# Kernel optimization log

Hardware: AMD Instinct MI355X
Metric: run time of the kernel (lower is better)

Reference implementation:

```python
import jax, jax.numpy as jnp
import numpy as np

LN_EPS = 1e-12  # BertLayerNorm default


def _digcn_forward(hidden_state, adjacency_matrix, Wl, bl, Ws, bs, Wr, br, ln_w, ln_b):
    B, S, D = hidden_state.shape
    temper = jnp.asarray(D, jnp.float32) ** 0.5
    i = jnp.arange(S)
    upper = (i[None, :] > i[:, None]).astype(hidden_state.dtype)  # strict upper: j > i
    lower = (i[None, :] < i[:, None]).astype(hidden_state.dtype)  # strict lower: j < i

    def layer(h, params):
        wl, b_l, ws, b_s, wr, b_r, g, beta = params
        # directed graph attention: softmax over full scores, then mask by adjacency and renormalize
        u = jnp.einsum('bid,bjd->bij', h, h) / temper            # [B,S,S]
        a = jax.nn.softmax(u, axis=-1)
        delta = a * adjacency_matrix
        attn = delta / (jnp.sum(delta, axis=-1, keepdims=True) + 1e-10)
        # three projections (torch Linear: x @ W.T + b)
        hl = h @ wl.T + b_l
        hs = h @ ws.T + b_s
        hr = h @ wr.T + b_r
        # split attention into strictly-upper (left), diagonal (self), strictly-lower (right)
        diag_a = jnp.diagonal(attn, axis1=1, axis2=2)            # [B,S]
        ctx = (jnp.einsum('bij,bjd->bid', attn * upper, hl)
               + diag_a[..., None] * hs
               + jnp.einsum('bij,bjd->bid', attn * lower, hr))
        # BertLayerNorm
        mean = ctx.mean(-1, keepdims=True)
        var = ctx.var(-1, keepdims=True)
        o = (ctx - mean) / jnp.sqrt(var + LN_EPS) * g + beta
        return jax.nn.relu(o), None

    out, _ = jax.lax.scan(layer, hidden_state, (Wl, bl, Ws, bs, Wr, br, ln_w, ln_b))
    return out


def setup_inputs() -> dict:
    key = jax.random.key(0)
    ks = jax.random.split(key, 6)
    B, S, D, L = 8, 1024, 768, 2
    scale = (1.0 / D) ** 0.5  # ~xavier scale for [D,D] linears
    hidden_state = jax.random.normal(ks[0], (B, S, D), jnp.float32)
    adjacency_matrix = (jax.random.uniform(ks[1], (B, S, S)) < 0.05).astype(jnp.float32)
    Wl = jax.random.normal(ks[2], (L, D, D), jnp.float32) * scale
    Ws = jax.random.normal(ks[3], (L, D, D), jnp.float32) * scale
    Wr = jax.random.normal(ks[4], (L, D, D), jnp.float32) * scale
    bl = jnp.zeros((L, D), jnp.float32)
    bs = jnp.zeros((L, D), jnp.float32)
    br = jnp.zeros((L, D), jnp.float32)
    ln_w = jnp.ones((L, D), jnp.float32)
    ln_b = jnp.zeros((L, D), jnp.float32)
    return dict(hidden_state=hidden_state, adjacency_matrix=adjacency_matrix,
                Wl=Wl, bl=bl, Ws=Ws, bs=bs, Wr=Wr, br=br, ln_w=ln_w, ln_b=ln_b)


def reference(hidden_state, adjacency_matrix, Wl, bl, Ws, bs, Wr, br, ln_w, ln_b):
    return _digcn_forward(hidden_state, adjacency_matrix, Wl, bl, Ws, bs, Wr, br, ln_w, ln_b)
```

## Files before the change

kernel.cpp:

```cpp
#include <hip/hip_runtime.h>
#include <hip/hip_bf16.h>


using bf16 = __hip_bfloat16;
typedef __attribute__((ext_vector_type(8))) short short8;
typedef __attribute__((ext_vector_type(4))) float f32x4;

#define B_ 8
#define S_ 1024
#define D_ 768
#define BS_ 8192
#define SS_ 1048576L
#define SD_ 786432L
#define DD_ 589824L

__device__ __forceinline__ void gload16(const void* g, void* l) {
  __builtin_amdgcn_global_load_lds((const __attribute__((address_space(1))) void*)g,
                                   (__attribute__((address_space(3))) void*)l, 16, 0, 0);
}

__device__ __forceinline__ f32x4 mfma16(short8 a, short8 b, f32x4 c) {
  return __builtin_amdgcn_mfma_f32_16x16x32_bf16(a, b, c, 0, 0, 0);
}

__device__ __forceinline__ float wave_sum(float v) {
  #pragma unroll
  for (int o = 32; o; o >>= 1) v += __shfl_xor(v, o);
  return v;
}

__device__ __forceinline__ void stage_tile(const bf16* g, long ld, int kt, short* s,
                                           int w, int lane) {
  #pragma unroll
  for (int i = 0; i < 4; ++i) {
    int rt = w * 32 + i * 8 + (lane >> 3);
    int ch = lane & 7;
    const bf16* src = g + (long)rt * ld + (long)kt * 64 + ((ch ^ (rt & 7)) << 3);
    gload16((const void*)src, (void*)(s + (w * 32 + i * 8) * 64));
  }
}

__device__ __forceinline__ short8 read_frag(const short* s, int r0, int kk, int lane) {
  int r = r0 + (lane & 15);
  int c = (kk << 2) + (lane >> 4);
  return *(const short8*)((const char*)s + r * 128 + ((c ^ (r & 7)) << 4));
}

__device__ __forceinline__ void compute_tile(const short* As, const short* Bs,
                                             f32x4 acc[4][4], int lane, int wm, int wn) {
  #pragma unroll
  for (int kk = 0; kk < 2; ++kk) {
    short8 af[4], bfr[4];
    #pragma unroll
    for (int m = 0; m < 4; ++m) af[m] = read_frag(As, wm * 64 + m * 16, kk, lane);
    #pragma unroll
    for (int n = 0; n < 4; ++n) bfr[n] = read_frag(Bs, wn * 64 + n * 16, kk, lane);
    #pragma unroll
    for (int m = 0; m < 4; ++m)
      #pragma unroll
      for (int n = 0; n < 4; ++n)
        acc[m][n] = mfma16(af[m], bfr[n], acc[m][n]);
  }
}

__device__ __forceinline__ void gemm_db(const bf16* A, long lda, const bf16* Bm, long ldb,
                                        int kt0, int kt1, short (*L)[8192],
                                        f32x4 acc[4][4], int w, int lane, int wm, int wn) {
  stage_tile(A, lda, kt0, L[0], w, lane);
  stage_tile(Bm, ldb, kt0, L[1], w, lane);
  asm volatile("s_waitcnt vmcnt(0)");
  __syncthreads();
  int cur = 0;
  for (int kt = kt0; kt < kt1; ++kt) {
    if (kt + 1 < kt1) {
      stage_tile(A, lda, kt + 1, L[2 * (cur ^ 1)], w, lane);
      stage_tile(Bm, ldb, kt + 1, L[2 * (cur ^ 1) + 1], w, lane);
    }
    compute_tile(L[2 * cur], L[2 * cur + 1], acc, lane, wm, wn);
    asm volatile("s_waitcnt vmcnt(0)");
    __syncthreads();
    cur ^= 1;
  }
}

__global__ __launch_bounds__(256) void k_scores(const bf16* __restrict__ hb,
                                                const float* __restrict__ adj,
                                                bf16* __restrict__ paU,
                                                bf16* __restrict__ paL,
                                                float* __restrict__ diagpa,
                                                float* __restrict__ Sm,
                                                float* __restrict__ Zs,
                                                float scale) {
  __shared__ short L[4][8192];
  int b = blockIdx.z;
  int tid = threadIdx.x, w = tid >> 6, lane = tid & 63, wm = w >> 1, wn = w & 1;
  const bf16* A = hb + (long)b * SD_ + (long)blockIdx.x * 128 * D_;
  const bf16* Bp = hb + (long)b * SD_ + (long)blockIdx.y * 128 * D_;
  f32x4 acc[4][4] = {};
  gemm_db(A, D_, Bp, D_, 0, 12, L, acc, w, lane, wm, wn);
  int row0 = blockIdx.x * 128 + wm * 64, col0 = blockIdx.y * 128 + wn * 64;
  #pragma unroll
  for (int m = 0; m < 4; ++m) {
    int rbase = row0 + m * 16 + ((lane >> 4) << 2);
    #pragma unroll
    for (int j = 0; j < 4; ++j) {
      int rs = rbase + j;
      long rowg = (long)b * S_ + rs;
      float psum = 0.f, pasum = 0.f;
      #pragma unroll
      for (int n = 0; n < 4; ++n) {
        int cs = col0 + n * 16 + (lane & 15);
        float p = __expf(acc[m][n][j] * scale);
        float a = adj[rowg * S_ + cs];
        bf16 pb = __float2bfloat16(p * a);
        float pa = __bfloat162float(pb);
        psum += p; pasum += pa;
        paU[rowg * S_ + cs] = (cs > rs) ? pb : __float2bfloat16(0.f);
        paL[rowg * S_ + cs] = (cs < rs) ? pb : __float2bfloat16(0.f);
        if (cs == rs) diagpa[rowg] = pa;
      }
      #pragma unroll
      for (int o = 1; o < 16; o <<= 1) {
        psum += __shfl_xor(psum, o);
        pasum += __shfl_xor(pasum, o);
      }
      if ((lane & 15) == 0) {
        atomicAdd(&Sm[rowg], pasum);
        atomicAdd(&Zs[rowg], psum);
      }
    }
  }
}

__global__ __launch_bounds__(256) void k_proj(const bf16* __restrict__ hb,
                                              const bf16* __restrict__ Wb,
                                              const float* __restrict__ bl,
                                              const float* __restrict__ bs,
                                              const float* __restrict__ br,
                                              bf16* __restrict__ hlT,
                                              bf16* __restrict__ hsb,
                                              bf16* __restrict__ hrT) {
  __shared__ short L[4][8192];
  int z = blockIdx.z;
  int tid = threadIdx.x, w = tid >> 6, lane = tid & 63, wm = w >> 1, wn = w & 1;
  const bf16* A = hb + (long)blockIdx.x * 128 * D_;
  const bf16* Bp = Wb + (long)z * 2 * DD_ + (long)blockIdx.y * 128 * D_;
  f32x4 acc[4][4] = {};
  gemm_db(A, D_, Bp, D_, 0, 12, L, acc, w, lane, wm, wn);
  const float* bias = (z == 0) ? bl : (z == 1) ? bs : br;
  int row0 = blockIdx.x * 128 + wm * 64, col0 = blockIdx.y * 128 + wn * 64;
  if (z == 1) {
    #pragma unroll
    for (int m = 0; m < 4; ++m) {
      int r = row0 + m * 16 + ((lane >> 4) << 2);
      #pragma unroll
      for (int n = 0; n < 4; ++n) {
        int c = col0 + n * 16 + (lane & 15);
        float bv = bias[c];
        #pragma unroll
        for (int j = 0; j < 4; ++j)
          hsb[(long)(r + j) * D_ + c] = __float2bfloat16(acc[m][n][j] + bv);
      }
    }
  } else {
    bf16* outT = (z == 0) ? hlT : hrT;
    #pragma unroll
    for (int m = 0; m < 4; ++m) {
      int r = row0 + m * 16 + ((lane >> 4) << 2);
      #pragma unroll
      for (int n = 0; n < 4; ++n) {
        int c = col0 + n * 16 + (lane & 15);
        float bv = bias[c];
        #pragma unroll
        for (int j = 0; j < 4; ++j)
          outT[(long)c * BS_ + r + j] = __float2bfloat16(acc[m][n][j] + bv);
      }
    }
  }
}

__global__ __launch_bounds__(256) void k_ctx(const bf16* __restrict__ paU,
                                             const bf16* __restrict__ paL,
                                             const bf16* __restrict__ hlT,
                                             const bf16* __restrict__ hrT,
                                             const bf16* __restrict__ hsb,
                                             const float* __restrict__ diagpa,
                                             const float* __restrict__ Sm,
                                             const float* __restrict__ Zs,
                                             float* __restrict__ ctx) {
  __shared__ short L[4][8192];
  int b = blockIdx.z;
  int tid = threadIdx.x, w = tid >> 6, lane = tid & 63, wm = w >> 1, wn = w & 1;
  int rm = blockIdx.x * 128;
  int t = rm >> 6;
  const bf16* A1 = paU + (long)b * SS_ + (long)rm * S_;
  const bf16* B1 = hlT + (long)blockIdx.y * 128 * BS_ + (long)b * S_;
  const bf16* A2 = paL + (long)b * SS_ + (long)rm * S_;
  const bf16* B2 = hrT + (long)blockIdx.y * 128 * BS_ + (long)b * S_;
  int ntU = 16 - t;
  int nt = ntU + t + 2;
  f32x4 acc[4][4] = {};

  const bf16 *Ap, *Bp; int kt;
  {
    Ap = A1; Bp = B1; kt = t;
    stage_tile(Ap, S_, kt, L[0], w, lane);
    stage_tile(Bp, BS_, kt, L[1], w, lane);
  }
  asm volatile("s_waitcnt vmcnt(0)");
  __syncthreads();
  int cur = 0;
  for (int q = 0; q < nt; ++q) {
    if (q + 1 < nt) {
      int qn = q + 1;
      if (qn < ntU) { Ap = A1; Bp = B1; kt = t + qn; }
      else          { Ap = A2; Bp = B2; kt = qn - ntU; }
      stage_tile(Ap, S_, kt, L[2 * (cur ^ 1)], w, lane);
      stage_tile(Bp, BS_, kt, L[2 * (cur ^ 1) + 1], w, lane);
    }
    compute_tile(L[2 * cur], L[2 * cur + 1], acc, lane, wm, wn);
    asm volatile("s_waitcnt vmcnt(0)");
    __syncthreads();
    cur ^= 1;
  }

  int row0 = rm + wm * 64, col0 = blockIdx.y * 128 + wn * 64;
  #pragma unroll
  for (int m = 0; m < 4; ++m) {
    int r = row0 + m * 16 + ((lane >> 4) << 2);
    float dg[4], inv[4];
    #pragma unroll
    for (int j = 0; j < 4; ++j) {
      long gr = (long)b * S_ + r + j;
      dg[j] = diagpa[gr];
      inv[j] = 1.0f / (Sm[gr] + 1e-10f * Zs[gr]);
    }
    #pragma unroll
    for (int n = 0; n < 4; ++n) {
      int c = col0 + n * 16 + (lane & 15);
      #pragma unroll
      for (int j = 0; j < 4; ++j) {
        long gr = (long)b * S_ + r + j;
        float hv = __bfloat162float(hsb[gr * D_ + c]);
        ctx[gr * D_ + c] = (acc[m][n][j] + dg[j] * hv) * inv[j];
      }
    }
  }
}

__global__ __launch_bounds__(256) void k_ln(const float* __restrict__ ctx,
                                            const float* __restrict__ g,
                                            const float* __restrict__ beta,
                                            float* __restrict__ outF,
                                            bf16* __restrict__ outB) {
  int wv = threadIdx.x >> 6, lane = threadIdx.x & 63;
  long row = (long)blockIdx.x * 4 + wv;
  const float* x = ctx + row * D_;
  float v[12]; float s = 0.f;
  #pragma unroll
  for (int k = 0; k < 12; ++k) { v[k] = x[k * 64 + lane]; s += v[k]; }
  s = wave_sum(s);
  float mean = s * (1.0f / 768.0f);
  float q = 0.f;
  #pragma unroll
  for (int k = 0; k < 12; ++k) { float d = v[k] - mean; q += d * d; }
  q = wave_sum(q);
  float inv = rsqrtf(fmaxf(q * (1.0f / 768.0f), 0.f) + 1e-12f);
  #pragma unroll
  for (int k = 0; k < 12; ++k) {
    int c = k * 64 + lane;
    float o = fmaxf((v[k] - mean) * inv * g[c] + beta[c], 0.f);
    if (outF) outF[row * D_ + c] = o;
    if (outB) outB[row * D_ + c] = __float2bfloat16(o);
  }
}

__global__ __launch_bounds__(256) void k_castf(const float* __restrict__ in,
                                               bf16* __restrict__ out) {
  long idx = ((long)blockIdx.x * 256 + threadIdx.x) * 4;
  float4 f = *(const float4*)(in + idx);
  out[idx] = __float2bfloat16(f.x);
  out[idx + 1] = __float2bfloat16(f.y);
  out[idx + 2] = __float2bfloat16(f.z);
  out[idx + 3] = __float2bfloat16(f.w);
}

__global__ __launch_bounds__(256) void k_castw(const float* __restrict__ wl,
                                               const float* __restrict__ ws_,
                                               const float* __restrict__ wr,
                                               bf16* __restrict__ out) {
  const float* src = (blockIdx.y == 0) ? wl : (blockIdx.y == 1) ? ws_ : wr;
  bf16* o = out + (long)blockIdx.y * 2 * DD_;
  long idx = ((long)blockIdx.x * 256 + threadIdx.x) * 4;
  float4 f = *(const float4*)(src + idx);
  o[idx] = __float2bfloat16(f.x);
  o[idx + 1] = __float2bfloat16(f.y);
  o[idx + 2] = __float2bfloat16(f.z);
  o[idx + 3] = __float2bfloat16(f.w);
}

extern "C" void kernel_launch(void* const* d_in, const int* in_sizes, int n_in,
                              void* d_out, int out_size, void* d_ws, size_t ws_size,
                              hipStream_t stream) {
  const float* hidden = (const float*)d_in[0];
  const float* adj    = (const float*)d_in[1];
  const float* Wl     = (const float*)d_in[2];
  const float* bl     = (const float*)d_in[3];
  const float* Ws     = (const float*)d_in[4];
  const float* bs     = (const float*)d_in[5];
  const float* Wr     = (const float*)d_in[6];
  const float* br     = (const float*)d_in[7];
  const float* lnw    = (const float*)d_in[8];
  const float* lnb    = (const float*)d_in[9];
  float* out = (float*)d_out;

  char* ws = (char*)d_ws;
  bf16*  hb     = (bf16*)(ws);
  bf16*  hlT    = (bf16*)(ws + 12582912);
  bf16*  hrT    = (bf16*)(ws + 25165824);
  bf16*  hsb    = (bf16*)(ws + 37748736);
  bf16*  Wb     = (bf16*)(ws + 50331648);
  float* diagpa = (float*)(ws + 57409536);
  float* SmZ    = (float*)(ws + 57442304);
  bf16*  paU    = (bf16*)(ws + 57507840);
  bf16*  paL    = (bf16*)(ws + 74285056);
  float* ctx    = (float*)(ws + 91062272);

  float* Sm = SmZ;
  float* Zs = SmZ + BS_;
  const float scale = 0.03608439182435161f;

  k_castf<<<6144, 256, 0, stream>>>(hidden, hb);
  k_castw<<<dim3(1152, 3), 256, 0, stream>>>(Wl, Ws, Wr, Wb);
  for (int l = 0; l < 2; ++l) {
    hipMemsetAsync(SmZ, 0, 2 * BS_ * sizeof(float), stream);
    k_scores<<<dim3(8, 8, B_), 256, 0, stream>>>(hb, adj, paU, paL, diagpa, Sm, Zs, scale);
    k_proj<<<dim3(64, 6, 3), 256, 0, stream>>>(hb, Wb + (long)l * DD_, bl + l * D_,
                                               bs + l * D_, br + l * D_, hlT, hsb, hrT);
    k_ctx<<<dim3(8, 6, B_), 256, 0, stream>>>(paU, paL, hlT, hrT, hsb, diagpa, Sm, Zs, ctx);
    k_ln<<<2048, 256, 0, stream>>>(ctx, lnw + l * D_, lnb + l * D_,
                                   (l == 1) ? out : nullptr,
                                   (l == 1) ? (bf16*)nullptr : hb);
  }
}
```

Before: 351.5 us.

## Bit-pack adjacency, merge masked attention buffers, drop row normalization, stage stores through LDS

A new kernel packs the float adjacency matrix into a bitmask once per call, and both layers reuse it. This replaces the float adjacency reads in the scores kernel. The scores kernel now writes one shared attention matrix, and only the diagonal 128x128 blocks get separate upper and lower copies. This replaces two full-size masked matrices. The per-row renormalization sums, their atomics and the memset are removed, because LayerNorm is invariant to a positive per-row scale; this leaves only a tiny epsilon difference. Output tiles in the scores and projection kernels are staged through shared memory so global stores, including the transposed ones, are coalesced 16-byte writes.

After: 353.9 us. Within noise of the previous version (+0.7%).

```diff
diff --git a/kernel.cpp b/kernel.cpp
--- a/kernel.cpp
+++ b/kernel.cpp
@@ -27,6 +27,11 @@
   #pragma unroll
   for (int o = 32; o; o >>= 1) v += __shfl_xor(v, o);
   return v;
+}
+
+__device__ __forceinline__ short bfbits(float x) {
+  bf16 h = __float2bfloat16(x);
+  return *reinterpret_cast<short*>(&h);
 }
 
 __device__ __forceinline__ void stage_tile(const bf16* g, long ld, int kt, short* s,
@@ -83,52 +88,79 @@
   }
 }
 
+__device__ __forceinline__ void copy_out(const short* T, short* dst, long ldg, int tid) {
+  #pragma unroll
+  for (int q = 0; q < 8; ++q) {
+    int id = q * 256 + tid;
+    int r = id >> 4, chk = id & 15;
+    short8 v = *(const short8*)(T + r * 136 + chk * 8);
+    *(short8*)(dst + (long)r * ldg + chk * 8) = v;
+  }
+}
+
+__global__ __launch_bounds__(256) void k_packadj(const float* __restrict__ adj,
+                                                 unsigned long long* __restrict__ am) {
+  int gw = (blockIdx.x * 256 + threadIdx.x) >> 6;
+  int lane = threadIdx.x & 63;
+  for (int it = 0; it < 64; ++it) {
+    long base = ((long)(it * 2048 + gw)) * 64;
+    float v = adj[base + lane];
+    unsigned long long b = __ballot(v != 0.0f);
+    if (lane == 0) am[base >> 6] = b;
+  }
+}
+
 __global__ __launch_bounds__(256) void k_scores(const bf16* __restrict__ hb,
-                                                const float* __restrict__ adj,
-                                                bf16* __restrict__ paU,
-                                                bf16* __restrict__ paL,
+                                                const unsigned* __restrict__ am,
+                                                bf16* __restrict__ pa,
+                                                bf16* __restrict__ paUb,
+                                                bf16* __restrict__ paLb,
                                                 float* __restrict__ diagpa,
-                                                float* __restrict__ Sm,
-                                                float* __restrict__ Zs,
                                                 float scale) {
   __shared__ short L[4][8192];
-  int b = blockIdx.z;
+  int b = blockIdx.z, bx = blockIdx.x, by = blockIdx.y;
   int tid = threadIdx.x, w = tid >> 6, lane = tid & 63, wm = w >> 1, wn = w & 1;
-  const bf16* A = hb + (long)b * SD_ + (long)blockIdx.x * 128 * D_;
-  const bf16* Bp = hb + (long)b * SD_ + (long)blockIdx.y * 128 * D_;
+  const bf16* A = hb + (long)b * SD_ + (long)bx * 128 * D_;
+  const bf16* Bp = hb + (long)b * SD_ + (long)by * 128 * D_;
   f32x4 acc[4][4] = {};
   gemm_db(A, D_, Bp, D_, 0, 12, L, acc, w, lane, wm, wn);
-  int row0 = blockIdx.x * 128 + wm * 64, col0 = blockIdx.y * 128 + wn * 64;
-  #pragma unroll
-  for (int m = 0; m < 4; ++m) {
-    int rbase = row0 + m * 16 + ((lane >> 4) << 2);
-    #pragma unroll
-    for (int j = 0; j < 4; ++j) {
-      int rs = rbase + j;
-      long rowg = (long)b * S_ + rs;
-      float psum = 0.f, pasum = 0.f;
+  bool dgb = (bx == by);
+  short* T = (short*)L;
+  int row0 = wm * 64, col0 = wn * 64;
+  int rs_off = bx * 128, cs_off = by * 128;
+  int npass = dgb ? 2 : 1;
+  for (int pass = 0; pass < npass; ++pass) {
+    if (pass) __syncthreads();
+    #pragma unroll
+    for (int m = 0; m < 4; ++m) {
+      int rl0 = row0 + m * 16 + ((lane >> 4) << 2);
       #pragma unroll
-      for (int n = 0; n < 4; ++n) {
-        int cs = col0 + n * 16 + (lane & 15);
-        float p = __expf(acc[m][n][j] * scale);
-        float a = adj[rowg * S_ + cs];
-        bf16 pb = __float2bfloat16(p * a);
-        float pa = __bfloat162float(pb);
-        psum += p; pasum += pa;
-        paU[rowg * S_ + cs] = (cs > rs) ? pb : __float2bfloat16(0.f);
-        paL[rowg * S_ + cs] = (cs < rs) ? pb : __float2bfloat16(0.f);
-        if (cs == rs) diagpa[rowg] = pa;
+      for (int j = 0; j < 4; ++j) {
+        int rl = rl0 + j;
+        int rglob = rs_off + rl;
+        long rowg = (long)b * S_ + rglob;
+        const unsigned* mrow = am + rowg * 32 + (cs_off >> 5) + (wn << 1);
+        unsigned w0 = mrow[0], w1 = mrow[1];
+        #pragma unroll
+        for (int n = 0; n < 4; ++n) {
+          int cl = col0 + n * 16 + (lane & 15);
+          int cglob = cs_off + cl;
+          unsigned wv = (n & 2) ? w1 : w0;
+          int bit = (wv >> (((n & 1) << 4) + (lane & 15))) & 1;
+          float p = __expf(acc[m][n][j] * scale);
+          float pav = bit ? p : 0.f;
+          if (dgb && pass == 0 && cglob == rglob) diagpa[rowg] = pav;
+          bool keep = !dgb || (pass == 0 ? (cglob > rglob) : (cglob < rglob));
+          T[rl * 136 + cl] = bfbits(keep ? pav : 0.f);
+        }
       }
-      #pragma unroll
-      for (int o = 1; o < 16; o <<= 1) {
-        psum += __shfl_xor(psum, o);
-        pasum += __shfl_xor(pasum, o);
-      }
-      if ((lane & 15) == 0) {
-        atomicAdd(&Sm[rowg], pasum);
-        atomicAdd(&Zs[rowg], psum);
-      }
-    }
+    }
+    __syncthreads();
+    short* dst; long ldg;
+    if (!dgb)           { dst = (short*)pa   + (long)b * SS_ + (long)rs_off * S_ + cs_off; ldg = S_; }
+    else if (pass == 0) { dst = (short*)paUb + (long)b * (S_ * 128L) + (long)rs_off * 128; ldg = 128; }
+    else                { dst = (short*)paLb + (long)b * (S_ * 128L) + (long)rs_off * 128; ldg = 128; }
+    copy_out(T, dst, ldg, tid);
   }
 }
 
@@ -148,75 +180,77 @@
   f32x4 acc[4][4] = {};
   gemm_db(A, D_, Bp, D_, 0, 12, L, acc, w, lane, wm, wn);
   const float* bias = (z == 0) ? bl : (z == 1) ? bs : br;
-  int row0 = blockIdx.x * 128 + wm * 64, col0 = blockIdx.y * 128 + wn * 64;
+  int rowg0 = blockIdx.x * 128, colg0 = blockIdx.y * 128;
+  short* T = (short*)L;
+  #pragma unroll
+  for (int m = 0; m < 4; ++m) {
+    int rl0 = wm * 64 + m * 16 + ((lane >> 4) << 2);
+    #pragma unroll
+    for (int n = 0; n < 4; ++n) {
+      int cl = wn * 64 + n * 16 + (lane & 15);
+      float bv = bias[colg0 + cl];
+      #pragma unroll
+      for (int j = 0; j < 4; ++j) {
+        short v = bfbits(acc[m][n][j] + bv);
+        if (z == 1) T[(rl0 + j) * 136 + cl] = v;
+        else        T[cl * 136 + rl0 + j] = v;
+      }
+    }
+  }
+  __syncthreads();
   if (z == 1) {
-    #pragma unroll
-    for (int m = 0; m < 4; ++m) {
-      int r = row0 + m * 16 + ((lane >> 4) << 2);
-      #pragma unroll
-      for (int n = 0; n < 4; ++n) {
-        int c = col0 + n * 16 + (lane & 15);
-        float bv = bias[c];
-        #pragma unroll
-        for (int j = 0; j < 4; ++j)
-          hsb[(long)(r + j) * D_ + c] = __float2bfloat16(acc[m][n][j] + bv);
-      }
-    }
+    copy_out(T, (short*)hsb + (long)rowg0 * D_ + colg0, D_, tid);
   } else {
-    bf16* outT = (z == 0) ? hlT : hrT;
-    #pragma unroll
-    for (int m = 0; m < 4; ++m) {
-      int r = row0 + m * 16 + ((lane >> 4) << 2);
-      #pragma unroll
-      for (int n = 0; n < 4; ++n) {
-        int c = col0 + n * 16 + (lane & 15);
-        float bv = bias[c];
-        #pragma unroll
-        for (int j = 0; j < 4; ++j)
-          outT[(long)c * BS_ + r + j] = __float2bfloat16(acc[m][n][j] + bv);
-      }
-    }
-  }
-}
-
-__global__ __launch_bounds__(256) void k_ctx(const bf16* __restrict__ paU,
-                                             const bf16* __restrict__ paL,
+    short* outT = (short*)((z == 0) ? hlT : hrT);
+    copy_out(T, outT + (long)colg0 * BS_ + rowg0, BS_, tid);
+  }
+}
+
+__global__ __launch_bounds__(256) void k_ctx(const bf16* __restrict__ pa,
+                                             const bf16* __restrict__ paUb,
+                                             const bf16* __restrict__ paLb,
                                              const bf16* __restrict__ hlT,
                                              const bf16* __restrict__ hrT,
                                              const bf16* __restrict__ hsb,
                                              const float* __restrict__ diagpa,
-                                             const float* __restrict__ Sm,
-                                             const float* __restrict__ Zs,
                                              float* __restrict__ ctx) {
   __shared__ short L[4][8192];
   int b = blockIdx.z;
   int tid = threadIdx.x, w = tid >> 6, lane = tid & 63, wm = w >> 1, wn = w & 1;
   int rm = blockIdx.x * 128;
-  int t = rm >> 6;
-  const bf16* A1 = paU + (long)b * SS_ + (long)rm * S_;
+  int t = rm >> 6, ntU = 16 - t, nt = ntU + t + 2;
+  const bf16* Af = pa + (long)b * SS_ + (long)rm * S_;
+  const bf16* Ub = paUb + (long)b * (S_ * 128L) + (long)rm * 128;
+  const bf16* Lb = paLb + (long)b * (S_ * 128L) + (long)rm * 128;
   const bf16* B1 = hlT + (long)blockIdx.y * 128 * BS_ + (long)b * S_;
-  const bf16* A2 = paL + (long)b * SS_ + (long)rm * S_;
   const bf16* B2 = hrT + (long)blockIdx.y * 128 * BS_ + (long)b * S_;
-  int ntU = 16 - t;
-  int nt = ntU + t + 2;
   f32x4 acc[4][4] = {};
 
-  const bf16 *Ap, *Bp; int kt;
-  {
-    Ap = A1; Bp = B1; kt = t;
-    stage_tile(Ap, S_, kt, L[0], w, lane);
-    stage_tile(Bp, BS_, kt, L[1], w, lane);
-  }
+  auto sel = [&](int q, const bf16*& Ap, long& la, int& kA, const bf16*& Bq, int& kB) {
+    if (q < ntU) {
+      int kt = t + q; Bq = B1; kB = kt;
+      if (q < 2) { Ap = Ub; la = 128; kA = q; }
+      else       { Ap = Af; la = S_;  kA = kt; }
+    } else {
+      int kt = q - ntU; Bq = B2; kB = kt;
+      if (kt < t) { Ap = Af; la = S_;  kA = kt; }
+      else        { Ap = Lb; la = 128; kA = kt - t; }
+    }
+  };
+
+  { const bf16 *Ap, *Bq; long la; int kA, kB;
+    sel(0, Ap, la, kA, Bq, kB);
+    stage_tile(Ap, la, kA, L[0], w, lane);
+    stage_tile(Bq, BS_, kB, L[1], w, lane); }
   asm volatile("s_waitcnt vmcnt(0)");
   __syncthreads();
   int cur = 0;
   for (int q = 0; q < nt; ++q) {
     if (q + 1 < nt) {
-      int qn = q + 1;
-      if (qn < ntU) { Ap = A1; Bp = B1; kt = t + qn; }
-      else          { Ap = A2; Bp = B2; kt = qn - ntU; }
-      stage_tile(Ap, S_, kt, L[2 * (cur ^ 1)], w, lane);
-      stage_tile(Bp, BS_, kt, L[2 * (cur ^ 1) + 1], w, lane);
+      const bf16 *Ap, *Bq; long la; int kA, kB;
+      sel(q + 1, Ap, la, kA, Bq, kB);
+      stage_tile(Ap, la, kA, L[2 * (cur ^ 1)], w, lane);
+      stage_tile(Bq, BS_, kB, L[2 * (cur ^ 1) + 1], w, lane);
     }
     compute_tile(L[2 * cur], L[2 * cur + 1], acc, lane, wm, wn);
     asm volatile("s_waitcnt vmcnt(0)");
@@ -228,13 +262,9 @@
   #pragma unroll
   for (int m = 0; m < 4; ++m) {
     int r = row0 + m * 16 + ((lane >> 4) << 2);
-    float dg[4], inv[4];
-    #pragma unroll
-    for (int j = 0; j < 4; ++j) {
-      long gr = (long)b * S_ + r + j;
-      dg[j] = diagpa[gr];
-      inv[j] = 1.0f / (Sm[gr] + 1e-10f * Zs[gr]);
-    }
+    float dg[4];
+    #pragma unroll
+    for (int j = 0; j < 4; ++j) dg[j] = diagpa[(long)b * S_ + r + j];
     #pragma unroll
     for (int n = 0; n < 4; ++n) {
       int c = col0 + n * 16 + (lane & 15);
@@ -242,7 +272,7 @@
       for (int j = 0; j < 4; ++j) {
         long gr = (long)b * S_ + r + j;
         float hv = __bfloat162float(hsb[gr * D_ + c]);
-        ctx[gr * D_ + c] = (acc[m][n][j] + dg[j] * hv) * inv[j];
+        ctx[gr * D_ + c] = acc[m][n][j] + dg[j] * hv;
       }
     }
   }
@@ -315,29 +345,28 @@
   float* out = (float*)d_out;
 
   char* ws = (char*)d_ws;
-  bf16*  hb     = (bf16*)(ws);
-  bf16*  hlT    = (bf16*)(ws + 12582912);
-  bf16*  hrT    = (bf16*)(ws + 25165824);
-  bf16*  hsb    = (bf16*)(ws + 37748736);
-  bf16*  Wb     = (bf16*)(ws + 50331648);
-  float* diagpa = (float*)(ws + 57409536);
-  float* SmZ    = (float*)(ws + 57442304);
-  bf16*  paU    = (bf16*)(ws + 57507840);
-  bf16*  paL    = (bf16*)(ws + 74285056);
-  float* ctx    = (float*)(ws + 91062272);
-
-  float* Sm = SmZ;
-  float* Zs = SmZ + BS_;
+  bf16*     hb     = (bf16*)(ws);
+  bf16*     hlT    = (bf16*)(ws + 12582912);
+  bf16*     hrT    = (bf16*)(ws + 25165824);
+  bf16*     hsb    = (bf16*)(ws + 37748736);
+  bf16*     Wb     = (bf16*)(ws + 50331648);
+  float*    diagpa = (float*)(ws + 57409536);
+  unsigned* amask  = (unsigned*)(ws + 57442304);
+  bf16*     pa     = (bf16*)(ws + 58490880);
+  bf16*     paUb   = (bf16*)(ws + 75268096);
+  bf16*     paLb   = (bf16*)(ws + 77365248);
+  float*    ctx    = (float*)(ws + 79462400);
+
   const float scale = 0.03608439182435161f;
 
   k_castf<<<6144, 256, 0, stream>>>(hidden, hb);
   k_castw<<<dim3(1152, 3), 256, 0, stream>>>(Wl, Ws, Wr, Wb);
+  k_packadj<<<512, 256, 0, stream>>>(adj, (unsigned long long*)amask);
   for (int l = 0; l < 2; ++l) {
-    hipMemsetAsync(SmZ, 0, 2 * BS_ * sizeof(float), stream);
-    k_scores<<<dim3(8, 8, B_), 256, 0, stream>>>(hb, adj, paU, paL, diagpa, Sm, Zs, scale);
+    k_scores<<<dim3(8, 8, B_), 256, 0, stream>>>(hb, amask, pa, paUb, paLb, diagpa, scale);
     k_proj<<<dim3(64, 6, 3), 256, 0, stream>>>(hb, Wb + (long)l * DD_, bl + l * D_,
                                                bs + l * D_, br + l * D_, hlT, hsb, hrT);
-    k_ctx<<<dim3(8, 6, B_), 256, 0, stream>>>(paU, paL, hlT, hrT, hsb, diagpa, Sm, Zs, ctx);
+    k_ctx<<<dim3(8, 6, B_), 256, 0, stream>>>(pa, paUb, paLb, hlT, hrT, hsb, diagpa, ctx);
     k_ln<<<2048, 256, 0, stream>>>(ctx, lnw + l * D_, lnb + l * D_,
                                    (l == 1) ? out : nullptr,
                                    (l == 1) ? (bf16*)nullptr : hb);
```
